# Kernel optimization log

Measured on AMD Instinct MI355X. Metric: run time of the kernel, lower is better.

## Reference

```python
import jax, jax.numpy as jnp
import numpy as np

BETA = 0.9      # leak factor
THR = 1.0       # snntorch Leaky default threshold
ALPHA = 2.0     # snntorch ATan surrogate default alpha

@jax.custom_vjp
def spike(x):
    # Heaviside fire; surrogate gradient (ATan) on backward, as in snntorch.
    return (x > 0).astype(x.dtype)

def _spike_fwd(x):
    return spike(x), x

def _spike_bwd(x, g):
    return (g * (ALPHA / 2.0) / (1.0 + (jnp.pi / 2.0 * ALPHA * x) ** 2),)

spike.defvjp(_spike_fwd, _spike_bwd)

def setup_inputs() -> dict:
    key = jax.random.key(0)
    ks = jax.random.split(key, 7)
    B, T, I, H, O = 512, 200, 784, 128, 10
    def lin(k, fan_out, fan_in):
        bound = 1.0 / np.sqrt(fan_in)
        return jax.random.uniform(k, (fan_out, fan_in), jnp.float32, -bound, bound)
    return {
        "x": jax.random.normal(ks[0], (B, T, I), jnp.float32),
        "W1": lin(ks[1], H, I), "b1": jax.random.uniform(ks[2], (H,), jnp.float32, -1/np.sqrt(I), 1/np.sqrt(I)),
        "W2": lin(ks[3], H, H), "b2": jax.random.uniform(ks[4], (H,), jnp.float32, -1/np.sqrt(H), 1/np.sqrt(H)),
        "W3": lin(ks[5], O, H), "b3": jax.random.uniform(ks[6], (O,), jnp.float32, -1/np.sqrt(H), 1/np.sqrt(H)),
    }

def reference(x, W1, b1, W2, b2, W3, b3):
    B = x.shape[0]
    H, O = W2.shape[0], W3.shape[0]
    xt = jnp.swapaxes(x, 0, 1)  # [T, B, I] for scan over time

    def lif(cur, mem, spk_prev):
        # snntorch Leaky (reset-by-subtraction, reset computed from previous mem):
        # mem_new = beta*mem + cur - spk_prev*thr ; spk = heaviside(mem_new - thr)
        mem = BETA * mem + cur - spk_prev * THR
        return spike(mem - THR), mem

    def step(carry, inp):
        m1, s1, m2, s2, m3, s3 = carry
        s1, m1 = lif(inp @ W1.T + b1, m1, s1)
        s2, m2 = lif(s1 @ W2.T + b2, m2, s2)
        s3, m3 = lif(s2 @ W3.T + b3, m3, s3)
        return (m1, s1, m2, s2, m3, s3), s3

    z = lambda d: jnp.zeros((B, d), x.dtype)
    init = (z(H), z(H), z(H), z(H), z(O), z(O))
    _, spk_rec = jax.lax.scan(step, init, xt)
    return spk_rec  # [T, B, num_outputs], matches torch.stack(spk_rec, dim=0)
```

## Files before the change

### kernel.cpp

```cpp
#include <hip/hip_runtime.h>

namespace {
constexpr int kB = 512;
constexpr int kT = 200;
constexpr int kI = 784;
constexpr int kH = 128;
constexpr int kO = 10;
constexpr int kM = kB * kT;
constexpr float kBeta = 0.9f;
constexpr float kThr = 1.0f;
constexpr int kSplitK0 = 400;
}

__global__ __launch_bounds__(256) void transposeW(const float* __restrict__ W,
                                                  float* __restrict__ WT,
                                                  int N, int K) {
  __shared__ float t[16][17];
  const int k0 = blockIdx.x * 16, n0 = blockIdx.y * 16;
  const int tx = threadIdx.x & 15, ty = threadIdx.x >> 4;
  t[ty][tx] = W[(size_t)(n0 + ty) * K + k0 + tx];
  __syncthreads();
  WT[(size_t)(k0 + ty) * N + n0 + tx] = t[tx][ty];
}

template <int KSTRIDE, int SPLIT>
__global__ __launch_bounds__(64, 4) void gemm64x64(
    const float* __restrict__ A, const float* __restrict__ BT,
    const float* __restrict__ bias, float* __restrict__ C, size_t coff) {
  constexpr int BK = 16;
  __shared__ float As[BK][68];
  __shared__ float Bs[BK][68];
  const int tid = threadIdx.x;
  const int tn = tid & 7;
  const int tm = tid >> 3;
  int mtile, n0, kbeg, nsteps;
  if (SPLIT) {
    mtile = blockIdx.x >> 2;
    n0 = ((blockIdx.x >> 1) & 1) * 64;
    const int half = blockIdx.x & 1;
    kbeg = half ? kSplitK0 : 0;
    nsteps = half ? (KSTRIDE - kSplitK0) / BK : kSplitK0 / BK;
    if (half) C += coff;
  } else {
    mtile = blockIdx.x >> 1;
    n0 = (blockIdx.x & 1) * 64;
    kbeg = 0;
    nsteps = KSTRIDE / BK;
  }
  const int row0 = mtile * 64;

  const int ar = tid >> 2;
  const int ac4 = (tid & 3) * 4;
  const int sbk = tid >> 4;
  const int sbn4 = (tid & 15) * 4;

  const float* aptr = A + (size_t)(row0 + ar) * KSTRIDE + kbeg + ac4;
  const float* btptr = BT + (size_t)(kbeg + sbk) * 128 + n0 + sbn4;

  float acc[8][8];
#pragma unroll
  for (int i = 0; i < 8; ++i)
#pragma unroll
    for (int j = 0; j < 8; ++j) acc[i][j] = 0.0f;

  for (int s = 0; s < nsteps; ++s) {
    const int k0 = s * BK;
    __syncthreads();
#pragma unroll
    for (int l = 0; l < 4; ++l) {
      const float4 va = *reinterpret_cast<const float4*>(
          aptr + (size_t)l * 16 * KSTRIDE + k0);
      const int r = ar + l * 16;
      As[ac4 + 0][r] = va.x; As[ac4 + 1][r] = va.y;
      As[ac4 + 2][r] = va.z; As[ac4 + 3][r] = va.w;
      const float4 vb = *reinterpret_cast<const float4*>(
          btptr + (size_t)(k0 + l * 4) * 128);
      *reinterpret_cast<float4*>(&Bs[sbk + l * 4][sbn4]) = vb;
    }
    __syncthreads();
#pragma unroll
    for (int kk = 0; kk < BK; ++kk) {
      float a[8], b[8];
      *reinterpret_cast<float4*>(&a[0]) =
          *reinterpret_cast<const float4*>(&As[kk][tm * 4]);
      *reinterpret_cast<float4*>(&a[4]) =
          *reinterpret_cast<const float4*>(&As[kk][32 + tm * 4]);
      *reinterpret_cast<float4*>(&b[0]) =
          *reinterpret_cast<const float4*>(&Bs[kk][tn * 4]);
      *reinterpret_cast<float4*>(&b[4]) =
          *reinterpret_cast<const float4*>(&Bs[kk][32 + tn * 4]);
#pragma unroll
      for (int i = 0; i < 8; ++i)
#pragma unroll
        for (int j = 0; j < 8; ++j) acc[i][j] = fmaf(a[i], b[j], acc[i][j]);
    }
  }

#pragma unroll
  for (int i = 0; i < 8; ++i) {
    const int m = (i < 4) ? (tm * 4 + i) : (32 + tm * 4 + (i - 4));
    const size_t r = (size_t)(row0 + m);
#pragma unroll
    for (int jh = 0; jh < 2; ++jh) {
      const int n = n0 + jh * 32 + tn * 4;
      float4 v;
      v.x = acc[i][jh * 4 + 0];
      v.y = acc[i][jh * 4 + 1];
      v.z = acc[i][jh * 4 + 2];
      v.w = acc[i][jh * 4 + 3];
      if (bias != nullptr) {
        v.x += bias[n + 0];
        v.y += bias[n + 1];
        v.z += bias[n + 2];
        v.w += bias[n + 3];
      }
      *reinterpret_cast<float4*>(&C[r * 128 + n]) = v;
    }
  }
}

#define LIF_STEP(mm, ss, curexpr)                                      \
  {                                                                    \
    const float cur_ = (curexpr);                                      \
    mm = __fsub_rn(__fadd_rn(__fmul_rn(kBeta, mm), cur_), ss);         \
    ss = (mm > kThr) ? 1.0f : 0.0f;                                    \
  }

__global__ __launch_bounds__(128) void lif_scan13(
    float* __restrict__ P0, const float* __restrict__ P1,
    const float* __restrict__ b1) {
  const int g = blockIdx.x * 128 + threadIdx.x;
  const int b = g >> 6;
  const int h2 = (g & 63) * 2;
  const size_t base = (size_t)b * kT * 128 + h2;
  const float bb0 = b1[h2], bb1 = b1[h2 + 1];
#define LD0(t) (*reinterpret_cast<const float2*>(&P0[base + (size_t)(t)*128]))
#define LD1(t) (*reinterpret_cast<const float2*>(&P1[base + (size_t)(t)*128]))
  float2 cA0 = LD0(0), cA1 = LD1(0), cB0 = LD0(1), cB1 = LD1(1);
  float2 cC0 = LD0(2), cC1 = LD1(2), cD0 = LD0(3), cD1 = LD1(3);
  float m0 = 0.f, m1 = 0.f, s0 = 0.f, s1 = 0.f;
  for (int t = 0; t < kT; t += 2) {
    const int pa = (t + 4 < kT) ? t + 4 : kT - 1;
    const int pb = (t + 5 < kT) ? t + 5 : kT - 1;
    const float2 nA0 = LD0(pa), nA1 = LD1(pa);
    const float2 nB0 = LD0(pb), nB1 = LD1(pb);
    LIF_STEP(m0, s0, __fadd_rn(__fadd_rn(cA0.x, cA1.x), bb0));
    LIF_STEP(m1, s1, __fadd_rn(__fadd_rn(cA0.y, cA1.y), bb1));
    *reinterpret_cast<float2*>(&P0[base + (size_t)t * 128]) =
        make_float2(s0, s1);
    LIF_STEP(m0, s0, __fadd_rn(__fadd_rn(cB0.x, cB1.x), bb0));
    LIF_STEP(m1, s1, __fadd_rn(__fadd_rn(cB0.y, cB1.y), bb1));
    *reinterpret_cast<float2*>(&P0[base + (size_t)(t + 1) * 128]) =
        make_float2(s0, s1);
    cA0 = cC0; cA1 = cC1; cB0 = cD0; cB1 = cD1;
    cC0 = nA0; cC1 = nA1; cD0 = nB0; cD1 = nB1;
  }
#undef LD0
#undef LD1
}

__global__ __launch_bounds__(128) void lif_scan2(float* __restrict__ buf) {
  const int g = blockIdx.x * 128 + threadIdx.x;
  const int b = g >> 6;
  const int h2 = (g & 63) * 2;
  const size_t base = (size_t)b * kT * 128 + h2;
#define LD(t) (*reinterpret_cast<const float2*>(&buf[base + (size_t)(t)*128]))
  float2 cA = LD(0), cB = LD(1), cC = LD(2), cD = LD(3);
  float m0 = 0.f, m1 = 0.f, s0 = 0.f, s1 = 0.f;
  for (int t = 0; t < kT; t += 2) {
    const int pa = (t + 4 < kT) ? t + 4 : kT - 1;
    const int pb = (t + 5 < kT) ? t + 5 : kT - 1;
    const float2 nA = LD(pa), nB = LD(pb);
    LIF_STEP(m0, s0, cA.x);
    LIF_STEP(m1, s1, cA.y);
    *reinterpret_cast<float2*>(&buf[base + (size_t)t * 128]) =
        make_float2(s0, s1);
    LIF_STEP(m0, s0, cB.x);
    LIF_STEP(m1, s1, cB.y);
    *reinterpret_cast<float2*>(&buf[base + (size_t)(t + 1) * 128]) =
        make_float2(s0, s1);
    cA = cC; cB = cD; cC = nA; cD = nB;
  }
#undef LD
}

__global__ __launch_bounds__(320) void gemm3_n10(
    const float* __restrict__ A, const float* __restrict__ W3,
    const float* __restrict__ b3, float* __restrict__ C) {
  __shared__ float Ss[64][132];
  __shared__ float Ws[10][132];
  __shared__ float bs[10];
  const int tid = threadIdx.x;
  const size_t row0 = (size_t)blockIdx.x * 64;

  {
    const int r = tid >> 5;
    const int c4 = (tid & 31) * 4;
    const float4 v = *reinterpret_cast<const float4*>(&W3[r * 128 + c4]);
    Ws[r][c4 + 0] = v.x;
    Ws[r][c4 + 1] = v.y;
    Ws[r][c4 + 2] = v.z;
    Ws[r][c4 + 3] = v.w;
    if (tid < 10) bs[tid] = b3[tid];
  }
  for (int fi = tid; fi < 2048; fi += 320) {
    const int r = fi >> 5;
    const int c4 = (fi & 31) * 4;
    const float4 v =
        *reinterpret_cast<const float4*>(&A[(row0 + r) * 128 + c4]);
    Ss[r][c4 + 0] = v.x;
    Ss[r][c4 + 1] = v.y;
    Ss[r][c4 + 2] = v.z;
    Ss[r][c4 + 3] = v.w;
  }
  __syncthreads();

#pragma unroll
  for (int l = 0; l < 2; ++l) {
    const int idx = tid + l * 320;
    const int r = idx / 10;
    const int o = idx - r * 10;
    float acc = bs[o];
#pragma unroll
    for (int k = 0; k < 128; k += 4) {
      const float4 a = *reinterpret_cast<const float4*>(&Ss[r][k]);
      const float4 w = *reinterpret_cast<const float4*>(&Ws[o][k]);
      acc = fmaf(a.x, w.x, acc);
      acc = fmaf(a.y, w.y, acc);
      acc = fmaf(a.z, w.z, acc);
      acc = fmaf(a.w, w.w, acc);
    }
    C[(row0 + r) * 10 + o] = acc;
  }
}

__global__ __launch_bounds__(256) void lif_scan_out(
    const float* __restrict__ cur3, float* __restrict__ out) {
  const int g = blockIdx.x * 256 + threadIdx.x;
  if (g >= kB * kO) return;
  const int b = g / kO;
  const int o = g - b * kO;
  float m = 0.0f, s = 0.0f;
#pragma unroll 4
  for (int t = 0; t < kT; ++t) {
    const float c = cur3[((size_t)b * kT + t) * kO + o];
    m = __fsub_rn(__fadd_rn(__fmul_rn(kBeta, m), c), s);
    s = (m > kThr) ? 1.0f : 0.0f;
    out[(size_t)t * (kB * kO) + g] = s;
  }
}

extern "C" void kernel_launch(void* const* d_in, const int* in_sizes, int n_in,
                              void* d_out, int out_size, void* d_ws,
                              size_t ws_size, hipStream_t stream) {
  (void)in_sizes;
  (void)n_in;
  (void)out_size;
  (void)ws_size;
  const float* x = (const float*)d_in[0];
  const float* W1 = (const float*)d_in[1];
  const float* b1 = (const float*)d_in[2];
  const float* W2 = (const float*)d_in[3];
  const float* b2 = (const float*)d_in[4];
  const float* W3 = (const float*)d_in[5];
  const float* b3 = (const float*)d_in[6];
  float* out = (float*)d_out;

  const size_t bufElems = (size_t)kM * kH;
  float* P0 = (float*)d_ws;
  float* P1 = P0 + bufElems;

  float* W1T = out;
  float* W2T = W1T + (size_t)kI * kH;

  transposeW<<<dim3(kI / 16, kH / 16), 256, 0, stream>>>(W1, W1T, kH, kI);
  transposeW<<<dim3(kH / 16, kH / 16), 256, 0, stream>>>(W2, W2T, kH, kH);

  gemm64x64<kI, 1><<<4 * (kM / 64), 64, 0, stream>>>(x, W1T, nullptr, P0,
                                                     bufElems);
  lif_scan13<<<256, 128, 0, stream>>>(P0, P1, b1);
  gemm64x64<kH, 0><<<2 * (kM / 64), 64, 0, stream>>>(P0, W2T, b2, P1, 0);
  lif_scan2<<<256, 128, 0, stream>>>(P1);
  gemm3_n10<<<kM / 64, 320, 0, stream>>>(P1, W3, b3, P0);
  lif_scan_out<<<(kB * kO + 255) / 256, 256, 0, stream>>>(P0, out);
}
```

Before: 411.4 us.

## Replace LDS-tiled GEMM with register-direct GEMM reading untransposed weights

```diff
diff --git a/kernel.cpp b/kernel.cpp
--- a/kernel.cpp
+++ b/kernel.cpp
@@ -9,53 +9,24 @@
 constexpr int kM = kB * kT;
 constexpr float kBeta = 0.9f;
 constexpr float kThr = 1.0f;
-constexpr int kSplitK0 = 400;
-}
-
-__global__ __launch_bounds__(256) void transposeW(const float* __restrict__ W,
-                                                  float* __restrict__ WT,
-                                                  int N, int K) {
-  __shared__ float t[16][17];
-  const int k0 = blockIdx.x * 16, n0 = blockIdx.y * 16;
-  const int tx = threadIdx.x & 15, ty = threadIdx.x >> 4;
-  t[ty][tx] = W[(size_t)(n0 + ty) * K + k0 + tx];
-  __syncthreads();
-  WT[(size_t)(k0 + ty) * N + n0 + tx] = t[tx][ty];
-}
-
-template <int KSTRIDE, int SPLIT>
-__global__ __launch_bounds__(64, 4) void gemm64x64(
-    const float* __restrict__ A, const float* __restrict__ BT,
-    const float* __restrict__ bias, float* __restrict__ C, size_t coff) {
-  constexpr int BK = 16;
-  __shared__ float As[BK][68];
-  __shared__ float Bs[BK][68];
+}
+
+template <int K>
+__global__ __launch_bounds__(64, 2) void gemm_reg64(
+    const float* __restrict__ A, const float* __restrict__ W,
+    const float* __restrict__ bias, float* __restrict__ C) {
+  constexpr int NG = K / 4;
   const int tid = threadIdx.x;
   const int tn = tid & 7;
   const int tm = tid >> 3;
-  int mtile, n0, kbeg, nsteps;
-  if (SPLIT) {
-    mtile = blockIdx.x >> 2;
-    n0 = ((blockIdx.x >> 1) & 1) * 64;
-    const int half = blockIdx.x & 1;
-    kbeg = half ? kSplitK0 : 0;
-    nsteps = half ? (KSTRIDE - kSplitK0) / BK : kSplitK0 / BK;
-    if (half) C += coff;
-  } else {
-    mtile = blockIdx.x >> 1;
-    n0 = (blockIdx.x & 1) * 64;
-    kbeg = 0;
-    nsteps = KSTRIDE / BK;
-  }
+  const int mtile = blockIdx.x >> 1;
+  const int n0 = (blockIdx.x & 1) * 64;
   const int row0 = mtile * 64;
 
-  const int ar = tid >> 2;
-  const int ac4 = (tid & 3) * 4;
-  const int sbk = tid >> 4;
-  const int sbn4 = (tid & 15) * 4;
-
-  const float* aptr = A + (size_t)(row0 + ar) * KSTRIDE + kbeg + ac4;
-  const float* btptr = BT + (size_t)(kbeg + sbk) * 128 + n0 + sbn4;
+  const float* A0 = A + (size_t)(row0 + tm * 4) * K;
+  const float* A1 = A + (size_t)(row0 + 32 + tm * 4) * K;
+  const float* W0 = W + (size_t)(n0 + tn * 4) * K;
+  const float* W1 = W + (size_t)(n0 + 32 + tn * 4) * K;
 
   float acc[8][8];
 #pragma unroll
@@ -63,38 +34,39 @@
 #pragma unroll
     for (int j = 0; j < 8; ++j) acc[i][j] = 0.0f;
 
-  for (int s = 0; s < nsteps; ++s) {
-    const int k0 = s * BK;
-    __syncthreads();
-#pragma unroll
-    for (int l = 0; l < 4; ++l) {
-      const float4 va = *reinterpret_cast<const float4*>(
-          aptr + (size_t)l * 16 * KSTRIDE + k0);
-      const int r = ar + l * 16;
-      As[ac4 + 0][r] = va.x; As[ac4 + 1][r] = va.y;
-      As[ac4 + 2][r] = va.z; As[ac4 + 3][r] = va.w;
-      const float4 vb = *reinterpret_cast<const float4*>(
-          btptr + (size_t)(k0 + l * 4) * 128);
-      *reinterpret_cast<float4*>(&Bs[sbk + l * 4][sbn4]) = vb;
-    }
-    __syncthreads();
-#pragma unroll
-    for (int kk = 0; kk < BK; ++kk) {
-      float a[8], b[8];
-      *reinterpret_cast<float4*>(&a[0]) =
-          *reinterpret_cast<const float4*>(&As[kk][tm * 4]);
-      *reinterpret_cast<float4*>(&a[4]) =
-          *reinterpret_cast<const float4*>(&As[kk][32 + tm * 4]);
-      *reinterpret_cast<float4*>(&b[0]) =
-          *reinterpret_cast<const float4*>(&Bs[kk][tn * 4]);
-      *reinterpret_cast<float4*>(&b[4]) =
-          *reinterpret_cast<const float4*>(&Bs[kk][32 + tn * 4]);
-#pragma unroll
-      for (int i = 0; i < 8; ++i)
-#pragma unroll
-        for (int j = 0; j < 8; ++j) acc[i][j] = fmaf(a[i], b[j], acc[i][j]);
-    }
-  }
+  float4 a0[8], b0[8], a1[8], b1[8];
+
+#define LOADG(aa, bb, g)                                                     \
+  {                                                                          \
+    const int k_ = (g) * 4;                                                  \
+    _Pragma("unroll") for (int i = 0; i < 4; ++i) {                          \
+      aa[i] = *reinterpret_cast<const float4*>(&A0[(size_t)i * K + k_]);     \
+      aa[i + 4] = *reinterpret_cast<const float4*>(&A1[(size_t)i * K + k_]); \
+      bb[i] = *reinterpret_cast<const float4*>(&W0[(size_t)i * K + k_]);     \
+      bb[i + 4] = *reinterpret_cast<const float4*>(&W1[(size_t)i * K + k_]); \
+    }                                                                        \
+  }
+
+#define COMPG(aa, bb)                                                        \
+  {                                                                          \
+    _Pragma("unroll") for (int i = 0; i < 8; ++i)                            \
+    _Pragma("unroll") for (int j = 0; j < 8; ++j) {                          \
+      acc[i][j] = fmaf(aa[i].x, bb[j].x, acc[i][j]);                         \
+      acc[i][j] = fmaf(aa[i].y, bb[j].y, acc[i][j]);                         \
+      acc[i][j] = fmaf(aa[i].z, bb[j].z, acc[i][j]);                         \
+      acc[i][j] = fmaf(aa[i].w, bb[j].w, acc[i][j]);                         \
+    }                                                                        \
+  }
+
+  LOADG(a0, b0, 0);
+  for (int g = 0; g < NG; g += 2) {
+    LOADG(a1, b1, g + 1);
+    COMPG(a0, b0);
+    if (g + 2 < NG) LOADG(a0, b0, g + 2);
+    COMPG(a1, b1);
+  }
+#undef LOADG
+#undef COMPG
 
 #pragma unroll
   for (int i = 0; i < 8; ++i) {
@@ -126,40 +98,7 @@
     ss = (mm > kThr) ? 1.0f : 0.0f;                                    \
   }
 
-__global__ __launch_bounds__(128) void lif_scan13(
-    float* __restrict__ P0, const float* __restrict__ P1,
-    const float* __restrict__ b1) {
-  const int g = blockIdx.x * 128 + threadIdx.x;
-  const int b = g >> 6;
-  const int h2 = (g & 63) * 2;
-  const size_t base = (size_t)b * kT * 128 + h2;
-  const float bb0 = b1[h2], bb1 = b1[h2 + 1];
-#define LD0(t) (*reinterpret_cast<const float2*>(&P0[base + (size_t)(t)*128]))
-#define LD1(t) (*reinterpret_cast<const float2*>(&P1[base + (size_t)(t)*128]))
-  float2 cA0 = LD0(0), cA1 = LD1(0), cB0 = LD0(1), cB1 = LD1(1);
-  float2 cC0 = LD0(2), cC1 = LD1(2), cD0 = LD0(3), cD1 = LD1(3);
-  float m0 = 0.f, m1 = 0.f, s0 = 0.f, s1 = 0.f;
-  for (int t = 0; t < kT; t += 2) {
-    const int pa = (t + 4 < kT) ? t + 4 : kT - 1;
-    const int pb = (t + 5 < kT) ? t + 5 : kT - 1;
-    const float2 nA0 = LD0(pa), nA1 = LD1(pa);
-    const float2 nB0 = LD0(pb), nB1 = LD1(pb);
-    LIF_STEP(m0, s0, __fadd_rn(__fadd_rn(cA0.x, cA1.x), bb0));
-    LIF_STEP(m1, s1, __fadd_rn(__fadd_rn(cA0.y, cA1.y), bb1));
-    *reinterpret_cast<float2*>(&P0[base + (size_t)t * 128]) =
-        make_float2(s0, s1);
-    LIF_STEP(m0, s0, __fadd_rn(__fadd_rn(cB0.x, cB1.x), bb0));
-    LIF_STEP(m1, s1, __fadd_rn(__fadd_rn(cB0.y, cB1.y), bb1));
-    *reinterpret_cast<float2*>(&P0[base + (size_t)(t + 1) * 128]) =
-        make_float2(s0, s1);
-    cA0 = cC0; cA1 = cC1; cB0 = cD0; cB1 = cD1;
-    cC0 = nA0; cC1 = nA1; cD0 = nB0; cD1 = nB1;
-  }
-#undef LD0
-#undef LD1
-}
-
-__global__ __launch_bounds__(128) void lif_scan2(float* __restrict__ buf) {
+__global__ __launch_bounds__(128) void lif_scan_h(float* __restrict__ buf) {
   const int g = blockIdx.x * 128 + threadIdx.x;
   const int b = g >> 6;
   const int h2 = (g & 63) * 2;
@@ -270,17 +209,10 @@
   float* P0 = (float*)d_ws;
   float* P1 = P0 + bufElems;
 
-  float* W1T = out;
-  float* W2T = W1T + (size_t)kI * kH;
-
-  transposeW<<<dim3(kI / 16, kH / 16), 256, 0, stream>>>(W1, W1T, kH, kI);
-  transposeW<<<dim3(kH / 16, kH / 16), 256, 0, stream>>>(W2, W2T, kH, kH);
-
-  gemm64x64<kI, 1><<<4 * (kM / 64), 64, 0, stream>>>(x, W1T, nullptr, P0,
-                                                     bufElems);
-  lif_scan13<<<256, 128, 0, stream>>>(P0, P1, b1);
-  gemm64x64<kH, 0><<<2 * (kM / 64), 64, 0, stream>>>(P0, W2T, b2, P1, 0);
-  lif_scan2<<<256, 128, 0, stream>>>(P1);
+  gemm_reg64<kI><<<2 * (kM / 64), 64, 0, stream>>>(x, W1, b1, P0);
+  lif_scan_h<<<256, 128, 0, stream>>>(P0);
+  gemm_reg64<kH><<<2 * (kM / 64), 64, 0, stream>>>(P0, W2, b2, P1);
+  lif_scan_h<<<256, 128, 0, stream>>>(P1);
   gemm3_n10<<<kM / 64, 320, 0, stream>>>(P1, W3, b3, P0);
   lif_scan_out<<<(kB * kO + 255) / 256, 256, 0, stream>>>(P0, out);
 }
```

After: 1.016 ms. +147.0%, slower.
